# Kernel optimization log

Measured on AMD Instinct MI355X. Metric: run time of the kernel, lower is better.

Reference implementation:

```python
import jax, jax.numpy as jnp
import numpy as np

N, E, IN_C, HID, H = 10000, 320000, 256, 128, 4
NEG_SLOPE = 0.2
BN_EPS = 1e-5


def setup_inputs() -> dict:
    key = jax.random.key(0)
    ks = jax.random.split(key, 16)
    s = lambda *shape: 1.0 / np.sqrt(shape[0])
    inp = {
        "x": jax.random.normal(ks[0], (N, IN_C), jnp.float32),
        "edge_index": jax.random.randint(ks[1], (2, E), 0, N, jnp.int64),
        # GATv2 layer 1 (in=256 -> H=4 heads of C=128, concat=False)
        "Wl1": jax.random.normal(ks[2], (IN_C, H * HID), jnp.float32) * s(IN_C),
        "Wr1": jax.random.normal(ks[3], (IN_C, H * HID), jnp.float32) * s(IN_C),
        "att1": jax.random.normal(ks[4], (H, HID), jnp.float32) * s(HID),
        "b1": jnp.zeros((HID,), jnp.float32),
        # GATv2 layer 2 (in=128 -> H=4 heads of C=128, concat=False)
        "Wl2": jax.random.normal(ks[5], (HID, H * HID), jnp.float32) * s(HID),
        "Wr2": jax.random.normal(ks[6], (HID, H * HID), jnp.float32) * s(HID),
        "att2": jax.random.normal(ks[7], (H, HID), jnp.float32) * s(HID),
        "b2": jnp.zeros((HID,), jnp.float32),
        # BatchNorm (inference mode: running stats)
        "g1": jnp.ones((HID,), jnp.float32),
        "be1": jnp.zeros((HID,), jnp.float32),
        "m1": jax.random.normal(ks[8], (HID,), jnp.float32) * 0.1,
        "v1": jnp.ones((HID,), jnp.float32),
        "g2": jnp.ones((HID,), jnp.float32),
        "be2": jnp.zeros((HID,), jnp.float32),
        "m2": jax.random.normal(ks[9], (HID,), jnp.float32) * 0.1,
        "v2": jnp.ones((HID,), jnp.float32),
        # Final Linear(hidden, 1)
        "Wlin": jax.random.normal(ks[10], (HID, 1), jnp.float32) * s(HID),
        "blin": jnp.zeros((1,), jnp.float32),
    }
    return inp


def _gatv2(x, src, dst, Wl, Wr, att, bias):
    """PyG GATv2Conv, heads=H, concat=False (mean over heads)."""
    n = x.shape[0]
    xl = (x @ Wl).reshape(n, H, HID)  # source-side projection
    xr = (x @ Wr).reshape(n, H, HID)  # target-side projection
    # per-edge GATv2 score: a^T LeakyReLU(Wl x_j + Wr x_i)
    e = jax.nn.leaky_relu(xl[src] + xr[dst], NEG_SLOPE)  # [E', H, C]
    logits = jnp.einsum("ehc,hc->eh", e, att)            # [E', H]
    # segment softmax over incoming edges of each dst node
    lmax = jax.ops.segment_max(logits, dst, num_segments=n)
    ex = jnp.exp(logits - lmax[dst])
    denom = jax.ops.segment_sum(ex, dst, num_segments=n)
    alpha = ex / (denom[dst] + 1e-16)                    # [E', H]
    # scatter-add weighted source features, then mean over heads
    out = jax.ops.segment_sum(alpha[:, :, None] * xl[src], dst, num_segments=n)
    return out.mean(axis=1) + bias, alpha


def _bn(x, g, b, m, v):
    return (x - m) * jax.lax.rsqrt(v + BN_EPS) * g + b


def reference(x, edge_index, Wl1, Wr1, att1, b1, Wl2, Wr2, att2, b2,
              g1, be1, m1, v1, g2, be2, m2, v2, Wlin, blin):
    n = x.shape[0]
    loops = jnp.arange(n, dtype=edge_index.dtype)
    src = jnp.concatenate([edge_index[0], loops])  # add_self_loops=True
    dst = jnp.concatenate([edge_index[1], loops])

    h, alpha1 = _gatv2(x, src, dst, Wl1, Wr1, att1, b1)
    h = jax.nn.relu(_bn(h, g1, be1, m1, v1))  # dropout = identity (eval)

    h, alpha2 = _gatv2(h, src, dst, Wl2, Wr2, att2, b2)
    h = jax.nn.relu(_bn(h, g2, be2, m2, v2))

    out = jax.nn.sigmoid(jax.nn.relu(h @ Wlin + blin))  # [N, 1]
    return out, alpha1, alpha2
```

## Files before the change

kernel.cpp:

```cpp
#include <hip/hip_runtime.h>
#include <hip/hip_bf16.h>

#define HID 128
#define NH  4
#define FEAT (NH*HID)
#define F2   (2*FEAT)
#define NEG_SLOPE 0.2f
#define BN_EPS 1e-5f
#define CAP  128

typedef __attribute__((ext_vector_type(8))) short bf16x8;
typedef __attribute__((ext_vector_type(4))) float f32x4;
typedef __attribute__((ext_vector_type(2))) float f32x2;

__device__ inline ushort f2bf(float f) {
    unsigned u = __float_as_uint(f);
    return (ushort)((u + 0x7fffu + ((u >> 16) & 1u)) >> 16);
}
__device__ inline void ubf8p(const ushort* p, f32x2* o) {
    uint4 q = *(const uint4*)p;
    o[0] = f32x2{__uint_as_float(q.x << 16), __uint_as_float(q.x & 0xffff0000u)};
    o[1] = f32x2{__uint_as_float(q.y << 16), __uint_as_float(q.y & 0xffff0000u)};
    o[2] = f32x2{__uint_as_float(q.z << 16), __uint_as_float(q.z & 0xffff0000u)};
    o[3] = f32x2{__uint_as_float(q.w << 16), __uint_as_float(q.w & 0xffff0000u)};
}

__global__ __launch_bounds__(256) void cast_bf16_deg(const float* __restrict__ in,
                                                     ushort* __restrict__ out, int n,
                                                     int* __restrict__ deg, int N)
{
    int gid = blockIdx.x * 256 + threadIdx.x;
    if (gid < N) deg[gid] = 0;
    int i = gid * 4;
    if (i >= n) return;
    float4 v = *(const float4*)(in + i);
    ushort4 o = make_ushort4(f2bf(v.x), f2bf(v.y), f2bf(v.z), f2bf(v.w));
    *(ushort4*)(out + i) = o;
}

__global__ __launch_bounds__(256) void transpose_cast4(const float* __restrict__ in0,
                                                       const float* __restrict__ in1,
                                                       const float* __restrict__ in2,
                                                       const float* __restrict__ in3,
                                                       ushort* __restrict__ out0,
                                                       ushort* __restrict__ out1,
                                                       ushort* __restrict__ out2,
                                                       ushort* __restrict__ out3,
                                                       int K01, int K23, int Nc)
{
    const int z = blockIdx.z;
    const float* in  = (z == 0) ? in0 : (z == 1) ? in1 : (z == 2) ? in2 : in3;
    ushort*      out = (z == 0) ? out0 : (z == 1) ? out1 : (z == 2) ? out2 : out3;
    const int K = (z < 2) ? K01 : K23;
    int bk = blockIdx.x * 32, bc = blockIdx.y * 32;
    if (bk >= K) return;
    __shared__ float t[32][33];
    int r = threadIdx.x >> 3, c4 = (threadIdx.x & 7) * 4;
    float4 v = *(const float4*)(in + (size_t)(bk + r) * Nc + bc + c4);
    t[r][c4 + 0] = v.x; t[r][c4 + 1] = v.y; t[r][c4 + 2] = v.z; t[r][c4 + 3] = v.w;
    __syncthreads();
    ushort4 o;
    o.x = f2bf(t[c4 + 0][r]); o.y = f2bf(t[c4 + 1][r]);
    o.z = f2bf(t[c4 + 2][r]); o.w = f2bf(t[c4 + 3][r]);
    *(ushort4*)(out + (size_t)(bc + r) * K + bk + c4) = o;
}

__global__ __launch_bounds__(256) void gemm_bf16(const ushort* __restrict__ A,
                                                 const ushort* __restrict__ Bt,
                                                 ushort* __restrict__ C,
                                                 int M, int Nc, int K)
{
    __shared__ __align__(16) ushort As[128 * 40];
    __shared__ __align__(16) ushort Bs[128 * 40];
    const int bm = blockIdx.x * 128;
    const int bn = blockIdx.y * 128;
    const int tid = threadIdx.x;
    const int wid = tid >> 6, lane = tid & 63;
    const int wr = wid >> 1, wc = wid & 1;
    const int l15 = lane & 15, l4 = lane >> 4;

    f32x4 acc[4][4] = {};

    for (int k0 = 0; k0 < K; k0 += 32) {
        #pragma unroll
        for (int s = 0; s < 2; ++s) {
            int c = tid + s * 256;
            int r = c >> 2, cc = (c & 3) * 8;
            uint4 v = make_uint4(0, 0, 0, 0);
            int gr = bm + r;
            if (gr < M) v = *(const uint4*)(A + (size_t)gr * K + k0 + cc);
            *(uint4*)&As[r * 40 + cc] = v;
            uint4 w = *(const uint4*)(Bt + (size_t)(bn + r) * K + k0 + cc);
            *(uint4*)&Bs[r * 40 + cc] = w;
        }
        __syncthreads();
        bf16x8 bfr[4];
        #pragma unroll
        for (int n = 0; n < 4; ++n)
            bfr[n] = *(const bf16x8*)&Bs[(wc * 64 + n * 16 + l15) * 40 + l4 * 8];
        #pragma unroll
        for (int m = 0; m < 4; ++m) {
            bf16x8 afr = *(const bf16x8*)&As[(wr * 64 + m * 16 + l15) * 40 + l4 * 8];
            #pragma unroll
            for (int n = 0; n < 4; ++n)
                acc[m][n] = __builtin_amdgcn_mfma_f32_16x16x32_bf16(afr, bfr[n], acc[m][n], 0, 0, 0);
        }
        __syncthreads();
    }
    #pragma unroll
    for (int m = 0; m < 4; ++m)
        #pragma unroll
        for (int n = 0; n < 4; ++n)
            #pragma unroll
            for (int r = 0; r < 4; ++r) {
                int row = bm + wr * 64 + m * 16 + l4 * 4 + r;
                int col = bn + wc * 64 + n * 16 + l15;
                if (row < M) C[(size_t)row * Nc + col] = f2bf(acc[m][n][r]);
            }
}

__global__ __launch_bounds__(256) void csr_count(const int* __restrict__ ei,
                                                 int* __restrict__ deg,
                                                 int E, int Etot)
{
    int i = blockIdx.x * 256 + threadIdx.x;
    if (i >= Etot) return;
    int dst = (i < E) ? ei[E + i] : (i - E);
    atomicAdd(&deg[dst], 1);
}

__global__ __launch_bounds__(1024) void scan_rowptr(const int* __restrict__ deg,
                                                    int* __restrict__ rowptr,
                                                    int* __restrict__ cursor,
                                                    int N)
{
    __shared__ int part[1024];
    int t = threadIdx.x;
    int chunk = (N + 1023) / 1024;
    int lo = t * chunk;
    int hi = lo + chunk; if (hi > N) hi = N; if (lo > N) lo = N;
    int s = 0;
    for (int i = lo; i < hi; ++i) s += deg[i];
    part[t] = s;
    __syncthreads();
    for (int off = 1; off < 1024; off <<= 1) {
        int v = (t >= off) ? part[t - off] : 0;
        __syncthreads();
        part[t] += v;
        __syncthreads();
    }
    int base = (t == 0) ? 0 : part[t - 1];
    for (int i = lo; i < hi; ++i) {
        rowptr[i] = base;
        cursor[i] = base;
        base += deg[i];
    }
    if (t == 1023) rowptr[N] = part[1023];
}

__global__ __launch_bounds__(256) void csr_fill(const int* __restrict__ ei,
                                                int* __restrict__ cursor,
                                                int* __restrict__ csr_src,
                                                int* __restrict__ csr_eid,
                                                int E, int Etot)
{
    int i = blockIdx.x * 256 + threadIdx.x;
    if (i >= Etot) return;
    int src, dst;
    if (i < E) { src = ei[i]; dst = ei[E + i]; }
    else       { src = dst = i - E; }
    int pos = atomicAdd(&cursor[dst], 1);
    csr_src[pos] = src;
    csr_eid[pos] = i;
}

template <bool FINAL>
__global__ __launch_bounds__(256) void fused_attn(const ushort* __restrict__ xlxr,
                                                  const int* __restrict__ rowptr,
                                                  const int* __restrict__ csr_src,
                                                  const int* __restrict__ csr_eid,
                                                  const float* __restrict__ att,
                                                  float* __restrict__ alpha,
                                                  const float* __restrict__ bias,
                                                  const float* __restrict__ g,
                                                  const float* __restrict__ be,
                                                  const float* __restrict__ bmn,
                                                  const float* __restrict__ bvr,
                                                  ushort* __restrict__ hout,
                                                  const float* __restrict__ Wlin,
                                                  const float* __restrict__ blin,
                                                  float* __restrict__ out, int N)
{
    __shared__ __align__(16) float lraw[4][CAP][NH];
    int n = (blockIdx.x * 256 + threadIdx.x) >> 6;
    int lane = threadIdx.x & 63;
    if (n >= N) return;
    const int wid = (threadIdx.x >> 6);
    int head = lane >> 4, sub = lane & 15;
    const size_t foff = (size_t)head * HID + sub * 8;

    f32x2 xr2[4], at2[4];
    ubf8p(xlxr + (size_t)n * F2 + FEAT + foff, xr2);
    {
        const float4* a4 = (const float4*)(att + foff);
        float4 t0 = a4[0], t1 = a4[1];
        at2[0] = f32x2{t0.x, t0.y}; at2[1] = f32x2{t0.z, t0.w};
        at2[2] = f32x2{t1.x, t1.y}; at2[3] = f32x2{t1.z, t1.w};
    }

    float mrun = -1e30f, den = 0.f;
    f32x2 acc2[4] = {};
    const int beg = rowptr[n], end = rowptr[n + 1];
    const int deg = end - beg;
    const bool big = deg > CAP;
    int k = beg;

    for (; k + 3 < end; k += 4) {
        int s0 = csr_src[k],     s1 = csr_src[k + 1];
        int s2 = csr_src[k + 2], s3 = csr_src[k + 3];

        f32x2 xv0[4], xv1[4], xv2[4], xv3[4];
        ubf8p(xlxr + (size_t)s0 * F2 + foff, xv0);
        ubf8p(xlxr + (size_t)s1 * F2 + foff, xv1);
        ubf8p(xlxr + (size_t)s2 * F2 + foff, xv2);
        ubf8p(xlxr + (size_t)s3 * F2 + foff, xv3);

        f32x2 p0 = {}, p1 = {}, p2 = {}, p3 = {};
        #pragma unroll
        for (int j = 0; j < 4; ++j) {
            f32x2 t0 = xv0[j] + xr2[j];
            f32x2 t1 = xv1[j] + xr2[j];
            f32x2 t2 = xv2[j] + xr2[j];
            f32x2 t3 = xv3[j] + xr2[j];
            f32x2 u0 = t0 * NEG_SLOPE, u1 = t1 * NEG_SLOPE;
            f32x2 u2 = t2 * NEG_SLOPE, u3 = t3 * NEG_SLOPE;
            t0.x = fmaxf(t0.x, u0.x); t0.y = fmaxf(t0.y, u0.y);
            t1.x = fmaxf(t1.x, u1.x); t1.y = fmaxf(t1.y, u1.y);
            t2.x = fmaxf(t2.x, u2.x); t2.y = fmaxf(t2.y, u2.y);
            t3.x = fmaxf(t3.x, u3.x); t3.y = fmaxf(t3.y, u3.y);
            p0 += t0 * at2[j]; p1 += t1 * at2[j];
            p2 += t2 * at2[j]; p3 += t3 * at2[j];
        }
        float l0 = p0.x + p0.y, l1 = p1.x + p1.y;
        float l2 = p2.x + p2.y, l3 = p3.x + p3.y;
        #pragma unroll
        for (int off = 1; off < 16; off <<= 1) {
            l0 += __shfl_xor(l0, off, 64);
            l1 += __shfl_xor(l1, off, 64);
            l2 += __shfl_xor(l2, off, 64);
            l3 += __shfl_xor(l3, off, 64);
        }
        if (!big) {
            if (sub == 0) {
                int kk = k - beg;
                lraw[wid][kk + 0][head] = l0;
                lraw[wid][kk + 1][head] = l1;
                lraw[wid][kk + 2][head] = l2;
                lraw[wid][kk + 3][head] = l3;
            }
        } else if (sub == 0) {
            alpha[(size_t)csr_eid[k]     * NH + head] = l0;
            alpha[(size_t)csr_eid[k + 1] * NH + head] = l1;
            alpha[(size_t)csr_eid[k + 2] * NH + head] = l2;
            alpha[(size_t)csr_eid[k + 3] * NH + head] = l3;
        }
        float bmax = fmaxf(fmaxf(l0, l1), fmaxf(l2, l3));
        if (bmax > mrun) {
            float sc = __expf(mrun - bmax);
            den *= sc;
            #pragma unroll
            for (int j = 0; j < 4; ++j) acc2[j] *= sc;
            mrun = bmax;
        }
        float w0 = __expf(l0 - mrun), w1 = __expf(l1 - mrun);
        float w2 = __expf(l2 - mrun), w3 = __expf(l3 - mrun);
        den += (w0 + w1) + (w2 + w3);
        #pragma unroll
        for (int j = 0; j < 4; ++j)
            acc2[j] += (w0 * xv0[j] + w1 * xv1[j]) + (w2 * xv2[j] + w3 * xv3[j]);
    }

    for (; k < end; ++k) {
        int src = csr_src[k];
        f32x2 xv[4];
        ubf8p(xlxr + (size_t)src * F2 + foff, xv);
        f32x2 ps = {};
        #pragma unroll
        for (int j = 0; j < 4; ++j) {
            f32x2 t = xv[j] + xr2[j];
            f32x2 u = t * NEG_SLOPE;
            t.x = fmaxf(t.x, u.x); t.y = fmaxf(t.y, u.y);
            ps += t * at2[j];
        }
        float s = ps.x + ps.y;
        #pragma unroll
        for (int off = 1; off < 16; off <<= 1) s += __shfl_xor(s, off, 64);
        if (!big) {
            if (sub == 0) lraw[wid][k - beg][head] = s;
        } else if (sub == 0) {
            alpha[(size_t)csr_eid[k] * NH + head] = s;
        }
        if (s > mrun) {
            float sc = __expf(mrun - s);
            den *= sc;
            #pragma unroll
            for (int j = 0; j < 4; ++j) acc2[j] *= sc;
            mrun = s;
        }
        float e = __expf(s - mrun);
        den += e;
        #pragma unroll
        for (int j = 0; j < 4; ++j) acc2[j] += e * xv[j];
    }

    float inv = 1.f / (den + 1e-16f);

    float t8[8];
    #pragma unroll
    for (int j = 0; j < 4; ++j) {
        float ta = acc2[j].x * inv;
        float tb = acc2[j].y * inv;
        ta += __shfl_xor(ta, 16, 64);
        ta += __shfl_xor(ta, 32, 64);
        tb += __shfl_xor(tb, 16, 64);
        tb += __shfl_xor(tb, 32, 64);
        t8[2 * j] = ta; t8[2 * j + 1] = tb;
    }
    if (head == 0) {
        float o[8];
        #pragma unroll
        for (int j = 0; j < 8; ++j) {
            int c = sub * 8 + j;
            float s = t8[j] * 0.25f + bias[c];
            float bn = (s - bmn[c]) * rsqrtf(bvr[c] + BN_EPS) * g[c] + be[c];
            o[j] = fmaxf(bn, 0.f);
        }
        if (FINAL) {
            float p = 0.f;
            #pragma unroll
            for (int j = 0; j < 8; ++j) p += o[j] * Wlin[sub * 8 + j];
            p += __shfl_xor(p, 1, 64);
            p += __shfl_xor(p, 2, 64);
            p += __shfl_xor(p, 4, 64);
            p += __shfl_xor(p, 8, 64);
            if (sub == 0) {
                float z = fmaxf(p + blin[0], 0.f);
                out[n] = 1.f / (1.f + __expf(-z));
            }
        } else {
            uint4 ov;
            unsigned w[4];
            #pragma unroll
            for (int q = 0; q < 4; ++q)
                w[q] = (unsigned)f2bf(o[2 * q]) | ((unsigned)f2bf(o[2 * q + 1]) << 16);
            ov.x = w[0]; ov.y = w[1]; ov.z = w[2]; ov.w = w[3];
            *(uint4*)(hout + (size_t)n * HID + sub * 8) = ov;
        }
    }

    float m_h[NH], i_h[NH];
    #pragma unroll
    for (int h = 0; h < NH; ++h) {
        m_h[h] = __shfl(mrun, h * 16, 64);
        float d = __shfl(den, h * 16, 64);
        i_h[h] = 1.f / (d + 1e-16f);
    }
    if (!big) {
        for (int e = lane; e < deg; e += 64) {
            int eid = csr_eid[beg + e];
            float4 r = *(const float4*)&lraw[wid][e][0];
            float4 o;
            o.x = __expf(r.x - m_h[0]) * i_h[0];
            o.y = __expf(r.y - m_h[1]) * i_h[1];
            o.z = __expf(r.z - m_h[2]) * i_h[2];
            o.w = __expf(r.w - m_h[3]) * i_h[3];
            *(float4*)&alpha[(size_t)eid * NH] = o;
        }
    } else {
        asm volatile("s_waitcnt vmcnt(0)" ::: "memory");
        float minv = i_h[head];
        for (int k2 = beg + sub; k2 < end; k2 += 16) {
            size_t idx = (size_t)csr_eid[k2] * NH + head;
            alpha[idx] = __expf(alpha[idx] - m_h[head]) * minv;
        }
    }
}

extern "C" void kernel_launch(void* const* d_in, const int* in_sizes, int n_in,
                              void* d_out, int out_size, void* d_ws, size_t ws_size,
                              hipStream_t stream)
{
    const float* x    = (const float*)d_in[0];
    const int*   ei   = (const int*)d_in[1];
    const float* Wl1  = (const float*)d_in[2];
    const float* Wr1  = (const float*)d_in[3];
    const float* att1 = (const float*)d_in[4];
    const float* b1   = (const float*)d_in[5];
    const float* Wl2  = (const float*)d_in[6];
    const float* Wr2  = (const float*)d_in[7];
    const float* att2 = (const float*)d_in[8];
    const float* b2   = (const float*)d_in[9];
    const float* g1   = (const float*)d_in[10];
    const float* be1  = (const float*)d_in[11];
    const float* m1   = (const float*)d_in[12];
    const float* v1   = (const float*)d_in[13];
    const float* g2   = (const float*)d_in[14];
    const float* be2  = (const float*)d_in[15];
    const float* m2   = (const float*)d_in[16];
    const float* v2   = (const float*)d_in[17];
    const float* Wlin = (const float*)d_in[18];
    const float* blin = (const float*)d_in[19];

    const int IN_C = 256;
    const int N = in_sizes[0] / IN_C;
    const int E = in_sizes[1] / 2;
    const int Etot = E + N;

    float* out    = (float*)d_out;
    float* alpha1 = out + N;
    float* alpha2 = alpha1 + (size_t)Etot * NH;

    char* wsb = (char*)d_ws;
    ushort* xbf   = (ushort*)wsb;                       wsb += (size_t)N * IN_C * 2;
    ushort* xlxr  = (ushort*)wsb;                       wsb += (size_t)N * F2 * 2;
    ushort* hbbf  = (ushort*)wsb;                       wsb += (size_t)N * HID * 2;
    ushort* wt1   = (ushort*)wsb;                       wsb += (size_t)F2 * IN_C * 2;
    ushort* wt2   = (ushort*)wsb;                       wsb += (size_t)F2 * HID * 2;
    int*    deg    = (int*)wsb;                         wsb += (size_t)N * 4;
    int*    cursor = (int*)wsb;                         wsb += (size_t)N * 4;
    int*    rowptr = (int*)wsb;                         wsb += (size_t)(N + 1) * 4;
    int*    csrsrc = (int*)wsb;                         wsb += (size_t)Etot * 4;
    int*    csreid = (int*)wsb;

    dim3 blk(256);
    dim3 gemm_grid((N + 127) / 128, F2 / 128);
    int node_wave_blocks = (N + 3) / 4;
    int etot_blocks = (Etot + 255) / 256;

    cast_bf16_deg<<<(N * IN_C / 4 + 255) / 256, blk, 0, stream>>>(x, xbf, N * IN_C, deg, N);
    transpose_cast4<<<dim3(IN_C / 32, FEAT / 32, 4), blk, 0, stream>>>(
        Wl1, Wr1, Wl2, Wr2,
        wt1, wt1 + (size_t)FEAT * IN_C, wt2, wt2 + (size_t)FEAT * HID,
        IN_C, HID, FEAT);

    csr_count<<<etot_blocks, blk, 0, stream>>>(ei, deg, E, Etot);
    scan_rowptr<<<1, 1024, 0, stream>>>(deg, rowptr, cursor, N);
    csr_fill<<<etot_blocks, blk, 0, stream>>>(ei, cursor, csrsrc, csreid, E, Etot);

    gemm_bf16<<<gemm_grid, blk, 0, stream>>>(xbf, wt1, xlxr, N, F2, IN_C);
    fused_attn<false><<<node_wave_blocks, blk, 0, stream>>>(xlxr, rowptr, csrsrc, csreid,
                                                            att1, alpha1, b1, g1, be1, m1, v1,
                                                            hbbf, Wlin, blin, out, N);

    gemm_bf16<<<gemm_grid, blk, 0, stream>>>(hbbf, wt2, xlxr, N, F2, HID);
    fused_attn<true><<<node_wave_blocks, blk, 0, stream>>>(xlxr, rowptr, csrsrc, csreid,
                                                           att2, alpha2, b2, g2, be2, m2, v2,
                                                           hbbf, Wlin, blin, out, N);
}
```

Before: 209.5 us.

## Split each node's edges across two waves and fuse x cast into GEMM

```diff
diff --git a/kernel.cpp b/kernel.cpp
--- a/kernel.cpp
+++ b/kernel.cpp
@@ -23,19 +23,6 @@
     o[1] = f32x2{__uint_as_float(q.y << 16), __uint_as_float(q.y & 0xffff0000u)};
     o[2] = f32x2{__uint_as_float(q.z << 16), __uint_as_float(q.z & 0xffff0000u)};
     o[3] = f32x2{__uint_as_float(q.w << 16), __uint_as_float(q.w & 0xffff0000u)};
-}
-
-__global__ __launch_bounds__(256) void cast_bf16_deg(const float* __restrict__ in,
-                                                     ushort* __restrict__ out, int n,
-                                                     int* __restrict__ deg, int N)
-{
-    int gid = blockIdx.x * 256 + threadIdx.x;
-    if (gid < N) deg[gid] = 0;
-    int i = gid * 4;
-    if (i >= n) return;
-    float4 v = *(const float4*)(in + i);
-    ushort4 o = make_ushort4(f2bf(v.x), f2bf(v.y), f2bf(v.z), f2bf(v.w));
-    *(ushort4*)(out + i) = o;
 }
 
 __global__ __launch_bounds__(256) void transpose_cast4(const float* __restrict__ in0,
@@ -65,7 +52,8 @@
     *(ushort4*)(out + (size_t)(bc + r) * K + bk + c4) = o;
 }
 
-__global__ __launch_bounds__(256) void gemm_bf16(const ushort* __restrict__ A,
+template <bool CVT>
+__global__ __launch_bounds__(256) void gemm_bf16(const void* __restrict__ Av,
                                                  const ushort* __restrict__ Bt,
                                                  ushort* __restrict__ C,
                                                  int M, int Nc, int K)
@@ -86,10 +74,25 @@
         for (int s = 0; s < 2; ++s) {
             int c = tid + s * 256;
             int r = c >> 2, cc = (c & 3) * 8;
-            uint4 v = make_uint4(0, 0, 0, 0);
             int gr = bm + r;
-            if (gr < M) v = *(const uint4*)(A + (size_t)gr * K + k0 + cc);
-            *(uint4*)&As[r * 40 + cc] = v;
+            if (CVT) {
+                const float* A = (const float*)Av;
+                float4 lo = make_float4(0.f, 0.f, 0.f, 0.f);
+                float4 hi = make_float4(0.f, 0.f, 0.f, 0.f);
+                if (gr < M) {
+                    lo = *(const float4*)(A + (size_t)gr * K + k0 + cc);
+                    hi = *(const float4*)(A + (size_t)gr * K + k0 + cc + 4);
+                }
+                ushort4 p0 = make_ushort4(f2bf(lo.x), f2bf(lo.y), f2bf(lo.z), f2bf(lo.w));
+                ushort4 p1 = make_ushort4(f2bf(hi.x), f2bf(hi.y), f2bf(hi.z), f2bf(hi.w));
+                *(ushort4*)&As[r * 40 + cc] = p0;
+                *(ushort4*)&As[r * 40 + cc + 4] = p1;
+            } else {
+                const ushort* A = (const ushort*)Av;
+                uint4 v = make_uint4(0, 0, 0, 0);
+                if (gr < M) v = *(const uint4*)(A + (size_t)gr * K + k0 + cc);
+                *(uint4*)&As[r * 40 + cc] = v;
+            }
             uint4 w = *(const uint4*)(Bt + (size_t)(bn + r) * K + k0 + cc);
             *(uint4*)&Bs[r * 40 + cc] = w;
         }
@@ -191,31 +194,41 @@
                                                   const float* __restrict__ blin,
                                                   float* __restrict__ out, int N)
 {
-    __shared__ __align__(16) float lraw[4][CAP][NH];
-    int n = (blockIdx.x * 256 + threadIdx.x) >> 6;
-    int lane = threadIdx.x & 63;
-    if (n >= N) return;
-    const int wid = (threadIdx.x >> 6);
-    int head = lane >> 4, sub = lane & 15;
+    __shared__ __align__(16) float lraw[2][CAP][NH];
+    __shared__ float accs[2][2][8][64];
+    __shared__ float smd[2][2][2][NH];
+    const int tid = threadIdx.x;
+    const int wid = tid >> 6;
+    const int lane = tid & 63;
+    const int nib = wid >> 1;
+    const int wv  = wid & 1;
+    const int n = blockIdx.x * 2 + nib;
+    const bool valid = n < N;
+    const int head = lane >> 4, sub = lane & 15;
     const size_t foff = (size_t)head * HID + sub * 8;
 
-    f32x2 xr2[4], at2[4];
-    ubf8p(xlxr + (size_t)n * F2 + FEAT + foff, xr2);
-    {
+    f32x2 xr2[4] = {}, at2[4] = {};
+    if (valid) {
+        ubf8p(xlxr + (size_t)n * F2 + FEAT + foff, xr2);
         const float4* a4 = (const float4*)(att + foff);
         float4 t0 = a4[0], t1 = a4[1];
         at2[0] = f32x2{t0.x, t0.y}; at2[1] = f32x2{t0.z, t0.w};
         at2[2] = f32x2{t1.x, t1.y}; at2[3] = f32x2{t1.z, t1.w};
     }
 
+    int beg = 0, end = 0;
+    if (valid) { beg = rowptr[n]; end = rowptr[n + 1]; }
+    const int deg = end - beg;
+    const bool big = deg > CAP;
+    const int half = (deg + 1) >> 1;
+    const int mybeg = beg + wv * half;
+    const int myend = wv ? end : (beg + half);
+
     float mrun = -1e30f, den = 0.f;
     f32x2 acc2[4] = {};
-    const int beg = rowptr[n], end = rowptr[n + 1];
-    const int deg = end - beg;
-    const bool big = deg > CAP;
-    int k = beg;
-
-    for (; k + 3 < end; k += 4) {
+    int k = mybeg;
+
+    for (; k + 3 < myend; k += 4) {
         int s0 = csr_src[k],     s1 = csr_src[k + 1];
         int s2 = csr_src[k + 2], s3 = csr_src[k + 3];
 
@@ -253,10 +266,10 @@
         if (!big) {
             if (sub == 0) {
                 int kk = k - beg;
-                lraw[wid][kk + 0][head] = l0;
-                lraw[wid][kk + 1][head] = l1;
-                lraw[wid][kk + 2][head] = l2;
-                lraw[wid][kk + 3][head] = l3;
+                lraw[nib][kk + 0][head] = l0;
+                lraw[nib][kk + 1][head] = l1;
+                lraw[nib][kk + 2][head] = l2;
+                lraw[nib][kk + 3][head] = l3;
             }
         } else if (sub == 0) {
             alpha[(size_t)csr_eid[k]     * NH + head] = l0;
@@ -280,7 +293,7 @@
             acc2[j] += (w0 * xv0[j] + w1 * xv1[j]) + (w2 * xv2[j] + w3 * xv3[j]);
     }
 
-    for (; k < end; ++k) {
+    for (; k < myend; ++k) {
         int src = csr_src[k];
         f32x2 xv[4];
         ubf8p(xlxr + (size_t)src * F2 + foff, xv);
@@ -296,7 +309,7 @@
         #pragma unroll
         for (int off = 1; off < 16; off <<= 1) s += __shfl_xor(s, off, 64);
         if (!big) {
-            if (sub == 0) lraw[wid][k - beg][head] = s;
+            if (sub == 0) lraw[nib][k - beg][head] = s;
         } else if (sub == 0) {
             alpha[(size_t)csr_eid[k] * NH + head] = s;
         }
@@ -313,75 +326,91 @@
         for (int j = 0; j < 4; ++j) acc2[j] += e * xv[j];
     }
 
-    float inv = 1.f / (den + 1e-16f);
-
-    float t8[8];
     #pragma unroll
     for (int j = 0; j < 4; ++j) {
-        float ta = acc2[j].x * inv;
-        float tb = acc2[j].y * inv;
-        ta += __shfl_xor(ta, 16, 64);
-        ta += __shfl_xor(ta, 32, 64);
-        tb += __shfl_xor(tb, 16, 64);
-        tb += __shfl_xor(tb, 32, 64);
-        t8[2 * j] = ta; t8[2 * j + 1] = tb;
-    }
-    if (head == 0) {
-        float o[8];
-        #pragma unroll
-        for (int j = 0; j < 8; ++j) {
-            int c = sub * 8 + j;
-            float s = t8[j] * 0.25f + bias[c];
-            float bn = (s - bmn[c]) * rsqrtf(bvr[c] + BN_EPS) * g[c] + be[c];
-            o[j] = fmaxf(bn, 0.f);
-        }
-        if (FINAL) {
-            float p = 0.f;
-            #pragma unroll
-            for (int j = 0; j < 8; ++j) p += o[j] * Wlin[sub * 8 + j];
-            p += __shfl_xor(p, 1, 64);
-            p += __shfl_xor(p, 2, 64);
-            p += __shfl_xor(p, 4, 64);
-            p += __shfl_xor(p, 8, 64);
-            if (sub == 0) {
-                float z = fmaxf(p + blin[0], 0.f);
-                out[n] = 1.f / (1.f + __expf(-z));
-            }
-        } else {
-            uint4 ov;
-            unsigned w[4];
-            #pragma unroll
-            for (int q = 0; q < 4; ++q)
-                w[q] = (unsigned)f2bf(o[2 * q]) | ((unsigned)f2bf(o[2 * q + 1]) << 16);
-            ov.x = w[0]; ov.y = w[1]; ov.z = w[2]; ov.w = w[3];
-            *(uint4*)(hout + (size_t)n * HID + sub * 8) = ov;
-        }
-    }
-
-    float m_h[NH], i_h[NH];
+        accs[nib][wv][2 * j][lane]     = acc2[j].x;
+        accs[nib][wv][2 * j + 1][lane] = acc2[j].y;
+    }
+    if (sub == 0) { smd[nib][wv][0][head] = mrun; smd[nib][wv][1][head] = den; }
+    __syncthreads();
+
+    float mh[NH], ih[NH];
     #pragma unroll
     for (int h = 0; h < NH; ++h) {
-        m_h[h] = __shfl(mrun, h * 16, 64);
-        float d = __shfl(den, h * 16, 64);
-        i_h[h] = 1.f / (d + 1e-16f);
-    }
-    if (!big) {
-        for (int e = lane; e < deg; e += 64) {
+        float a0 = smd[nib][0][0][h], a1 = smd[nib][1][0][h];
+        float mg = fmaxf(a0, a1);
+        float d = smd[nib][0][1][h] * __expf(a0 - mg) + smd[nib][1][1][h] * __expf(a1 - mg);
+        mh[h] = mg; ih[h] = 1.f / (d + 1e-16f);
+    }
+
+    if (valid && wv == 0) {
+        float m0 = smd[nib][0][0][head], m1 = smd[nib][1][0][head];
+        float mg = fmaxf(m0, m1);
+        float e0h = __expf(m0 - mg), e1h = __expf(m1 - mg);
+        float dg = smd[nib][0][1][head] * e0h + smd[nib][1][1][head] * e1h;
+        float invh = 1.f / (dg + 1e-16f);
+        float t8[8];
+        #pragma unroll
+        for (int j = 0; j < 8; ++j) {
+            float t = (accs[nib][0][j][lane] * e0h + accs[nib][1][j][lane] * e1h) * invh;
+            t += __shfl_xor(t, 16, 64);
+            t += __shfl_xor(t, 32, 64);
+            t8[j] = t;
+        }
+        if (head == 0) {
+            float o[8];
+            #pragma unroll
+            for (int j = 0; j < 8; ++j) {
+                int c = sub * 8 + j;
+                float s = t8[j] * 0.25f + bias[c];
+                float bn = (s - bmn[c]) * rsqrtf(bvr[c] + BN_EPS) * g[c] + be[c];
+                o[j] = fmaxf(bn, 0.f);
+            }
+            if (FINAL) {
+                float p = 0.f;
+                #pragma unroll
+                for (int j = 0; j < 8; ++j) p += o[j] * Wlin[sub * 8 + j];
+                p += __shfl_xor(p, 1, 64);
+                p += __shfl_xor(p, 2, 64);
+                p += __shfl_xor(p, 4, 64);
+                p += __shfl_xor(p, 8, 64);
+                if (sub == 0) {
+                    float z = fmaxf(p + blin[0], 0.f);
+                    out[n] = 1.f / (1.f + __expf(-z));
+                }
+            } else {
+                uint4 ov;
+                unsigned w[4];
+                #pragma unroll
+                for (int q = 0; q < 4; ++q)
+                    w[q] = (unsigned)f2bf(o[2 * q]) | ((unsigned)f2bf(o[2 * q + 1]) << 16);
+                ov.x = w[0]; ov.y = w[1]; ov.z = w[2]; ov.w = w[3];
+                *(uint4*)(hout + (size_t)n * HID + sub * 8) = ov;
+            }
+        }
+    }
+
+    if (valid && !big) {
+        for (int e = (mybeg - beg) + lane; e < (myend - beg); e += 64) {
             int eid = csr_eid[beg + e];
-            float4 r = *(const float4*)&lraw[wid][e][0];
+            float4 r = *(const float4*)&lraw[nib][e][0];
             float4 o;
-            o.x = __expf(r.x - m_h[0]) * i_h[0];
-            o.y = __expf(r.y - m_h[1]) * i_h[1];
-            o.z = __expf(r.z - m_h[2]) * i_h[2];
-            o.w = __expf(r.w - m_h[3]) * i_h[3];
+            o.x = __expf(r.x - mh[0]) * ih[0];
+            o.y = __expf(r.y - mh[1]) * ih[1];
+            o.z = __expf(r.z - mh[2]) * ih[2];
+            o.w = __expf(r.w - mh[3]) * ih[3];
             *(float4*)&alpha[(size_t)eid * NH] = o;
         }
-    } else {
+    } else if (valid) {
         asm volatile("s_waitcnt vmcnt(0)" ::: "memory");
-        float minv = i_h[head];
-        for (int k2 = beg + sub; k2 < end; k2 += 16) {
+        float m0 = smd[nib][0][0][head], m1 = smd[nib][1][0][head];
+        float mg = fmaxf(m0, m1);
+        float dg = smd[nib][0][1][head] * __expf(m0 - mg) +
+                   smd[nib][1][1][head] * __expf(m1 - mg);
+        float invh = 1.f / (dg + 1e-16f);
+        for (int k2 = mybeg + sub; k2 < myend; k2 += 16) {
             size_t idx = (size_t)csr_eid[k2] * NH + head;
-            alpha[idx] = __expf(alpha[idx] - m_h[head]) * minv;
+            alpha[idx] = __expf(alpha[idx] - mg) * invh;
         }
     }
 }
@@ -421,7 +450,6 @@
     float* alpha2 = alpha1 + (size_t)Etot * NH;
 
     char* wsb = (char*)d_ws;
-    ushort* xbf   = (ushort*)wsb;                       wsb += (size_t)N * IN_C * 2;
     ushort* xlxr  = (ushort*)wsb;                       wsb += (size_t)N * F2 * 2;
     ushort* hbbf  = (ushort*)wsb;                       wsb += (size_t)N * HID * 2;
     ushort* wt1   = (ushort*)wsb;                       wsb += (size_t)F2 * IN_C * 2;
@@ -434,26 +462,25 @@
 
     dim3 blk(256);
     dim3 gemm_grid((N + 127) / 128, F2 / 128);
-    int node_wave_blocks = (N + 3) / 4;
+    int attn_blocks = (N + 1) / 2;
     int etot_blocks = (Etot + 255) / 256;
 
-    cast_bf16_deg<<<(N * IN_C / 4 + 255) / 256, blk, 0, stream>>>(x, xbf, N * IN_C, deg, N);
+    hipMemsetAsync(deg, 0, (size_t)N * sizeof(int), stream);
     transpose_cast4<<<dim3(IN_C / 32, FEAT / 32, 4), blk, 0, stream>>>(
         Wl1, Wr1, Wl2, Wr2,
         wt1, wt1 + (size_t)FEAT * IN_C, wt2, wt2 + (size_t)FEAT * HID,
         IN_C, HID, FEAT);
-
     csr_count<<<etot_blocks, blk, 0, stream>>>(ei, deg, E, Etot);
     scan_rowptr<<<1, 1024, 0, stream>>>(deg, rowptr, cursor, N);
     csr_fill<<<etot_blocks, blk, 0, stream>>>(ei, cursor, csrsrc, csreid, E, Etot);
 
-    gemm_bf16<<<gemm_grid, blk, 0, stream>>>(xbf, wt1, xlxr, N, F2, IN_C);
-    fused_attn<false><<<node_wave_blocks, blk, 0, stream>>>(xlxr, rowptr, csrsrc, csreid,
-                                                            att1, alpha1, b1, g1, be1, m1, v1,
-                                                            hbbf, Wlin, blin, out, N);
-
-    gemm_bf16<<<gemm_grid, blk, 0, stream>>>(hbbf, wt2, xlxr, N, F2, HID);
-    fused_attn<true><<<node_wave_blocks, blk, 0, stream>>>(xlxr, rowptr, csrsrc, csreid,
-                                                           att2, alpha2, b2, g2, be2, m2, v2,
-                                                           hbbf, Wlin, blin, out, N);
-}
+    gemm_bf16<true><<<gemm_grid, blk, 0, stream>>>(x, wt1, xlxr, N, F2, IN_C);
+    fused_attn<false><<<attn_blocks, blk, 0, stream>>>(xlxr, rowptr, csrsrc, csreid,
+                                                       att1, alpha1, b1, g1, be1, m1, v1,
+                                                       hbbf, Wlin, blin, out, N);
+
+    gemm_bf16<false><<<gemm_grid, blk, 0, stream>>>(hbbf, wt2, xlxr, N, F2, HID);
+    fused_attn<true><<<attn_blocks, blk, 0, stream>>>(xlxr, rowptr, csrsrc, csreid,
+                                                      att2, alpha2, b2, g2, be2, m2, v2,
+                                                      hbbf, Wlin, blin, out, N);
+}
```

Result: slower. 221.3 us (+5.7%).

## Fuse x cast into layer-1 GEMM and merge prep kernels into horizontal launches

Applied to the files above, without the earlier changes.

```diff
diff --git a/kernel.cpp b/kernel.cpp
--- a/kernel.cpp
+++ b/kernel.cpp
@@ -25,35 +25,86 @@
     o[3] = f32x2{__uint_as_float(q.w << 16), __uint_as_float(q.w & 0xffff0000u)};
 }
 
-__global__ __launch_bounds__(256) void cast_bf16_deg(const float* __restrict__ in,
-                                                     ushort* __restrict__ out, int n,
-                                                     int* __restrict__ deg, int N)
-{
-    int gid = blockIdx.x * 256 + threadIdx.x;
-    if (gid < N) deg[gid] = 0;
-    int i = gid * 4;
-    if (i >= n) return;
-    float4 v = *(const float4*)(in + i);
-    ushort4 o = make_ushort4(f2bf(v.x), f2bf(v.y), f2bf(v.z), f2bf(v.w));
-    *(ushort4*)(out + i) = o;
-}
-
-__global__ __launch_bounds__(256) void transpose_cast4(const float* __restrict__ in0,
-                                                       const float* __restrict__ in1,
-                                                       const float* __restrict__ in2,
-                                                       const float* __restrict__ in3,
-                                                       ushort* __restrict__ out0,
-                                                       ushort* __restrict__ out1,
-                                                       ushort* __restrict__ out2,
-                                                       ushort* __restrict__ out3,
-                                                       int K01, int K23, int Nc)
-{
-    const int z = blockIdx.z;
-    const float* in  = (z == 0) ? in0 : (z == 1) ? in1 : (z == 2) ? in2 : in3;
-    ushort*      out = (z == 0) ? out0 : (z == 1) ? out1 : (z == 2) ? out2 : out3;
-    const int K = (z < 2) ? K01 : K23;
-    int bk = blockIdx.x * 32, bc = blockIdx.y * 32;
-    if (bk >= K) return;
+template <bool CVT>
+__device__ inline void gemm_body(const void* __restrict__ Av,
+                                 const ushort* __restrict__ Bt,
+                                 ushort* __restrict__ C,
+                                 int M, int Nc, int K, int bm, int bn)
+{
+    __shared__ __align__(16) ushort As[128 * 40];
+    __shared__ __align__(16) ushort Bs[128 * 40];
+    const int tid = threadIdx.x;
+    const int wid = tid >> 6, lane = tid & 63;
+    const int wr = wid >> 1, wc = wid & 1;
+    const int l15 = lane & 15, l4 = lane >> 4;
+
+    f32x4 acc[4][4] = {};
+
+    for (int k0 = 0; k0 < K; k0 += 32) {
+        #pragma unroll
+        for (int s = 0; s < 2; ++s) {
+            int c = tid + s * 256;
+            int r = c >> 2, cc = (c & 3) * 8;
+            int gr = bm + r;
+            if (CVT) {
+                const float* A = (const float*)Av;
+                float4 lo = make_float4(0.f, 0.f, 0.f, 0.f);
+                float4 hi = make_float4(0.f, 0.f, 0.f, 0.f);
+                if (gr < M) {
+                    lo = *(const float4*)(A + (size_t)gr * K + k0 + cc);
+                    hi = *(const float4*)(A + (size_t)gr * K + k0 + cc + 4);
+                }
+                ushort4 p0 = make_ushort4(f2bf(lo.x), f2bf(lo.y), f2bf(lo.z), f2bf(lo.w));
+                ushort4 p1 = make_ushort4(f2bf(hi.x), f2bf(hi.y), f2bf(hi.z), f2bf(hi.w));
+                *(ushort4*)&As[r * 40 + cc] = p0;
+                *(ushort4*)&As[r * 40 + cc + 4] = p1;
+            } else {
+                const ushort* A = (const ushort*)Av;
+                uint4 v = make_uint4(0, 0, 0, 0);
+                if (gr < M) v = *(const uint4*)(A + (size_t)gr * K + k0 + cc);
+                *(uint4*)&As[r * 40 + cc] = v;
+            }
+            uint4 w = *(const uint4*)(Bt + (size_t)(bn + r) * K + k0 + cc);
+            *(uint4*)&Bs[r * 40 + cc] = w;
+        }
+        __syncthreads();
+        bf16x8 bfr[4];
+        #pragma unroll
+        for (int n = 0; n < 4; ++n)
+            bfr[n] = *(const bf16x8*)&Bs[(wc * 64 + n * 16 + l15) * 40 + l4 * 8];
+        #pragma unroll
+        for (int m = 0; m < 4; ++m) {
+            bf16x8 afr = *(const bf16x8*)&As[(wr * 64 + m * 16 + l15) * 40 + l4 * 8];
+            #pragma unroll
+            for (int n = 0; n < 4; ++n)
+                acc[m][n] = __builtin_amdgcn_mfma_f32_16x16x32_bf16(afr, bfr[n], acc[m][n], 0, 0, 0);
+        }
+        __syncthreads();
+    }
+    #pragma unroll
+    for (int m = 0; m < 4; ++m)
+        #pragma unroll
+        for (int n = 0; n < 4; ++n)
+            #pragma unroll
+            for (int r = 0; r < 4; ++r) {
+                int row = bm + wr * 64 + m * 16 + l4 * 4 + r;
+                int col = bn + wc * 64 + n * 16 + l15;
+                if (row < M) C[(size_t)row * Nc + col] = f2bf(acc[m][n][r]);
+            }
+}
+
+__global__ __launch_bounds__(256) void gemm_bf16(const ushort* __restrict__ A,
+                                                 const ushort* __restrict__ Bt,
+                                                 ushort* __restrict__ C,
+                                                 int M, int Nc, int K)
+{
+    gemm_body<false>(A, Bt, C, M, Nc, K, blockIdx.x * 128, blockIdx.y * 128);
+}
+
+__device__ inline void transpose_body(const float* __restrict__ in,
+                                      ushort* __restrict__ out,
+                                      int K, int Nc, int bk, int bc)
+{
     __shared__ float t[32][33];
     int r = threadIdx.x >> 3, c4 = (threadIdx.x & 7) * 4;
     float4 v = *(const float4*)(in + (size_t)(bk + r) * Nc + bc + c4);
@@ -65,68 +116,61 @@
     *(ushort4*)(out + (size_t)(bc + r) * K + bk + c4) = o;
 }
 
-__global__ __launch_bounds__(256) void gemm_bf16(const ushort* __restrict__ A,
-                                                 const ushort* __restrict__ Bt,
-                                                 ushort* __restrict__ C,
-                                                 int M, int Nc, int K)
-{
-    __shared__ __align__(16) ushort As[128 * 40];
-    __shared__ __align__(16) ushort Bs[128 * 40];
-    const int bm = blockIdx.x * 128;
-    const int bn = blockIdx.y * 128;
-    const int tid = threadIdx.x;
-    const int wid = tid >> 6, lane = tid & 63;
-    const int wr = wid >> 1, wc = wid & 1;
-    const int l15 = lane & 15, l4 = lane >> 4;
-
-    f32x4 acc[4][4] = {};
-
-    for (int k0 = 0; k0 < K; k0 += 32) {
-        #pragma unroll
-        for (int s = 0; s < 2; ++s) {
-            int c = tid + s * 256;
-            int r = c >> 2, cc = (c & 3) * 8;
-            uint4 v = make_uint4(0, 0, 0, 0);
-            int gr = bm + r;
-            if (gr < M) v = *(const uint4*)(A + (size_t)gr * K + k0 + cc);
-            *(uint4*)&As[r * 40 + cc] = v;
-            uint4 w = *(const uint4*)(Bt + (size_t)(bn + r) * K + k0 + cc);
-            *(uint4*)&Bs[r * 40 + cc] = w;
-        }
-        __syncthreads();
-        bf16x8 bfr[4];
-        #pragma unroll
-        for (int n = 0; n < 4; ++n)
-            bfr[n] = *(const bf16x8*)&Bs[(wc * 64 + n * 16 + l15) * 40 + l4 * 8];
-        #pragma unroll
-        for (int m = 0; m < 4; ++m) {
-            bf16x8 afr = *(const bf16x8*)&As[(wr * 64 + m * 16 + l15) * 40 + l4 * 8];
-            #pragma unroll
-            for (int n = 0; n < 4; ++n)
-                acc[m][n] = __builtin_amdgcn_mfma_f32_16x16x32_bf16(afr, bfr[n], acc[m][n], 0, 0, 0);
-        }
-        __syncthreads();
-    }
-    #pragma unroll
-    for (int m = 0; m < 4; ++m)
-        #pragma unroll
-        for (int n = 0; n < 4; ++n)
-            #pragma unroll
-            for (int r = 0; r < 4; ++r) {
-                int row = bm + wr * 64 + m * 16 + l4 * 4 + r;
-                int col = bn + wc * 64 + n * 16 + l15;
-                if (row < M) C[(size_t)row * Nc + col] = f2bf(acc[m][n][r]);
-            }
-}
-
-__global__ __launch_bounds__(256) void csr_count(const int* __restrict__ ei,
-                                                 int* __restrict__ deg,
-                                                 int E, int Etot)
-{
-    int i = blockIdx.x * 256 + threadIdx.x;
-    if (i >= Etot) return;
-    int dst = (i < E) ? ei[E + i] : (i - E);
-    atomicAdd(&deg[dst], 1);
+__global__ __launch_bounds__(256) void prep_a(const float* __restrict__ Wl1,
+                                              const float* __restrict__ Wr1,
+                                              const float* __restrict__ Wl2,
+                                              const float* __restrict__ Wr2,
+                                              ushort* __restrict__ o0,
+                                              ushort* __restrict__ o1,
+                                              ushort* __restrict__ o2,
+                                              ushort* __restrict__ o3,
+                                              int IN_C,
+                                              const int* __restrict__ ei,
+                                              int* __restrict__ deg,
+                                              int E, int Etot)
+{
+    const int b = blockIdx.x;
+    if (b < 384) {
+        int z, idx;
+        if (b < 256) { z = b >> 7; idx = b & 127; }
+        else         { z = 2 + ((b - 256) >> 6); idx = (b - 256) & 63; }
+        const float* in  = (z == 0) ? Wl1 : (z == 1) ? Wr1 : (z == 2) ? Wl2 : Wr2;
+        ushort*      out = (z == 0) ? o0  : (z == 1) ? o1  : (z == 2) ? o2  : o3;
+        const int K = (z < 2) ? IN_C : HID;
+        int bx = (z < 2) ? (idx & 7) : (idx & 3);
+        int by = (z < 2) ? (idx >> 3) : (idx >> 2);
+        transpose_body(in, out, K, FEAT, bx * 32, by * 32);
+    } else {
+        int i = (b - 384) * 256 + threadIdx.x;
+        if (i >= Etot) return;
+        int dst = (i < E) ? ei[E + i] : (i - E);
+        atomicAdd(&deg[dst], 1);
+    }
+}
+
+__global__ __launch_bounds__(256) void prep_b(const float* __restrict__ x,
+                                              const ushort* __restrict__ wt1,
+                                              ushort* __restrict__ xlxr,
+                                              int M, int Nc, int K, int nbx, int GB,
+                                              const int* __restrict__ ei,
+                                              int* __restrict__ cursor,
+                                              int* __restrict__ csr_src,
+                                              int* __restrict__ csr_eid,
+                                              int E, int Etot)
+{
+    const int b = blockIdx.x;
+    if (b < GB) {
+        gemm_body<true>(x, wt1, xlxr, M, Nc, K, (b % nbx) * 128, (b / nbx) * 128);
+    } else {
+        int i = (b - GB) * 256 + threadIdx.x;
+        if (i >= Etot) return;
+        int src, dst;
+        if (i < E) { src = ei[i]; dst = ei[E + i]; }
+        else       { src = dst = i - E; }
+        int pos = atomicAdd(&cursor[dst], 1);
+        csr_src[pos] = src;
+        csr_eid[pos] = i;
+    }
 }
 
 __global__ __launch_bounds__(1024) void scan_rowptr(const int* __restrict__ deg,
@@ -156,22 +200,6 @@
         base += deg[i];
     }
     if (t == 1023) rowptr[N] = part[1023];
-}
-
-__global__ __launch_bounds__(256) void csr_fill(const int* __restrict__ ei,
-                                                int* __restrict__ cursor,
-                                                int* __restrict__ csr_src,
-                                                int* __restrict__ csr_eid,
-                                                int E, int Etot)
-{
-    int i = blockIdx.x * 256 + threadIdx.x;
-    if (i >= Etot) return;
-    int src, dst;
-    if (i < E) { src = ei[i]; dst = ei[E + i]; }
-    else       { src = dst = i - E; }
-    int pos = atomicAdd(&cursor[dst], 1);
-    csr_src[pos] = src;
-    csr_eid[pos] = i;
 }
 
 template <bool FINAL>
@@ -421,7 +449,6 @@
     float* alpha2 = alpha1 + (size_t)Etot * NH;
 
     char* wsb = (char*)d_ws;
-    ushort* xbf   = (ushort*)wsb;                       wsb += (size_t)N * IN_C * 2;
     ushort* xlxr  = (ushort*)wsb;                       wsb += (size_t)N * F2 * 2;
     ushort* hbbf  = (ushort*)wsb;                       wsb += (size_t)N * HID * 2;
     ushort* wt1   = (ushort*)wsb;                       wsb += (size_t)F2 * IN_C * 2;
@@ -433,26 +460,29 @@
     int*    csreid = (int*)wsb;
 
     dim3 blk(256);
-    dim3 gemm_grid((N + 127) / 128, F2 / 128);
+    const int nbx = (N + 127) / 128;
+    const int GB  = nbx * (F2 / 128);
+    const int etot_blocks = (Etot + 255) / 256;
     int node_wave_blocks = (N + 3) / 4;
-    int etot_blocks = (Etot + 255) / 256;
-
-    cast_bf16_deg<<<(N * IN_C / 4 + 255) / 256, blk, 0, stream>>>(x, xbf, N * IN_C, deg, N);
-    transpose_cast4<<<dim3(IN_C / 32, FEAT / 32, 4), blk, 0, stream>>>(
+
+    hipMemsetAsync(deg, 0, (size_t)N * sizeof(int), stream);
+
+    prep_a<<<384 + etot_blocks, blk, 0, stream>>>(
         Wl1, Wr1, Wl2, Wr2,
         wt1, wt1 + (size_t)FEAT * IN_C, wt2, wt2 + (size_t)FEAT * HID,
-        IN_C, HID, FEAT);
-
-    csr_count<<<etot_blocks, blk, 0, stream>>>(ei, deg, E, Etot);
+        IN_C, ei, deg, E, Etot);
+
     scan_rowptr<<<1, 1024, 0, stream>>>(deg, rowptr, cursor, N);
-    csr_fill<<<etot_blocks, blk, 0, stream>>>(ei, cursor, csrsrc, csreid, E, Etot);
-
-    gemm_bf16<<<gemm_grid, blk, 0, stream>>>(xbf, wt1, xlxr, N, F2, IN_C);
+
+    prep_b<<<GB + etot_blocks, blk, 0, stream>>>(
+        x, wt1, xlxr, N, F2, IN_C, nbx, GB,
+        ei, cursor, csrsrc, csreid, E, Etot);
+
     fused_attn<false><<<node_wave_blocks, blk, 0, stream>>>(xlxr, rowptr, csrsrc, csreid,
                                                             att1, alpha1, b1, g1, be1, m1, v1,
                                                             hbbf, Wlin, blin, out, N);
 
-    gemm_bf16<<<gemm_grid, blk, 0, stream>>>(hbbf, wt2, xlxr, N, F2, HID);
+    gemm_bf16<<<dim3(nbx, F2 / 128), blk, 0, stream>>>(hbbf, wt2, xlxr, N, F2, HID);
     fused_attn<true><<<node_wave_blocks, blk, 0, stream>>>(xlxr, rowptr, csrsrc, csreid,
                                                            att2, alpha2, b2, g2, be2, m2, v2,
                                                            hbbf, Wlin, blin, out, N);
```

New measurement: 195.9 us. 1.07x faster.
